# Kernel optimization log

Measured on AMD Instinct MI355X. Metric: run time of the kernel, lower is better.

The kernel has to match this reference:

```python
import jax, jax.numpy as jnp
import numpy as np
import math

B, N, F_IN, F_OUT = 16, 2048, 256, 64


def setup_inputs() -> dict:
    key = jax.random.key(0)
    k1, k2, k3, k4 = jax.random.split(key, 4)
    x = jax.random.normal(k1, (B, N, F_IN), dtype=jnp.float32)
    adj = jax.random.randint(k2, (B, N, N), 0, 2, dtype=jnp.int32)
    stdv = 1.0 / math.sqrt(F_OUT)
    weight = jax.random.uniform(k3, (F_IN, F_OUT), dtype=jnp.float32, minval=-stdv, maxval=stdv)
    # weight2 stdv = 1/sqrt(1) = 1.0
    weight2 = jax.random.uniform(k4, (2 * F_OUT, 1), dtype=jnp.float32, minval=-1.0, maxval=1.0)
    return {"x": x, "adj": adj, "weight": weight, "weight2": weight2}


def reference(x, adj, weight, weight2):
    # h[b,n,o] = (x @ weight)  -- shared linear projection
    h = jnp.einsum("bni,io->bno", x, weight)
    Fo = weight.shape[1]
    # Split additive-attention vector: e_ij = relu(h_i . a_src + h_j . a_dst)
    # Mathematically identical to cat([h_i, h_j]) @ weight2 of the original.
    a_src = weight2[:Fo, 0]
    a_dst = weight2[Fo:, 0]
    s_src = jnp.einsum("bno,o->bn", h, a_src)  # [B, N]
    s_dst = jnp.einsum("bno,o->bn", h, a_dst)  # [B, N]
    e = jax.nn.relu(s_src[:, :, None] + s_dst[:, None, :])  # [B, N, N]
    NEG = jnp.float32(-9e15)
    scores = jnp.where(adj > 0, e, NEG)
    attention = jax.nn.softmax(scores, axis=2)  # softmax over neighbors j
    # dropout = 0.0 / eval mode -> identity
    out = jnp.einsum("bij,bjo->bio", attention, h)  # [B, N, F_OUT]
    return out
```

## Files before the change

kernel.cpp:

```cpp
#include <hip/hip_runtime.h>
#include <hip/hip_bf16.h>

#define BB 16
#define NN 2048
#define FIN 256
#define FO 64
#define CH 128
#define HSTR 136

typedef __bf16 bf16x8 __attribute__((ext_vector_type(8)));
typedef float  f32x4  __attribute__((ext_vector_type(4)));
typedef int    i32x4  __attribute__((ext_vector_type(4)));

__global__ __launch_bounds__(256) void k1_gemm(
    const float* __restrict__ x, const float* __restrict__ weight,
    const float* __restrict__ w2,
    __bf16* __restrict__ hT, float* __restrict__ s_src, float* __restrict__ s_dst) {
    __shared__ __bf16 WtL[FO * 264];
    __shared__ float vsL[FIN], vdL[FIN];
    int t = threadIdx.x;
    {
        const float4* wr = (const float4*)(weight + t * FO);
        float a = 0.f, d = 0.f;
#pragma unroll
        for (int c = 0; c < 16; ++c) {
            float4 v = wr[c];
            int o = c * 4;
            WtL[(o + 0) * 264 + t] = (__bf16)v.x;
            WtL[(o + 1) * 264 + t] = (__bf16)v.y;
            WtL[(o + 2) * 264 + t] = (__bf16)v.z;
            WtL[(o + 3) * 264 + t] = (__bf16)v.w;
            a += v.x * w2[o] + v.y * w2[o + 1] + v.z * w2[o + 2] + v.w * w2[o + 3];
            d += v.x * w2[FO + o] + v.y * w2[FO + o + 1] +
                 v.z * w2[FO + o + 2] + v.w * w2[FO + o + 3];
        }
        vsL[t] = a;
        vdL[t] = d;
    }
    __syncthreads();

    int lane = threadIdx.x & 63, w = threadIdx.x >> 6;
    int quad = lane >> 4, m = lane & 15;
    int Rbase = blockIdx.x * 64 + w * 16;
    int R = Rbase + m;
    const float* xr = x + (long)R * FIN;

    f32x4 acc[4] = {};
    float ps = 0.f, pd = 0.f;

#pragma unroll
    for (int k0 = 0; k0 < FIN; k0 += 32) {
        int kb = k0 + quad * 8;
        float4 x0 = *(const float4*)(xr + kb);
        float4 x1 = *(const float4*)(xr + kb + 4);
        float4 u0 = *(const float4*)(vsL + kb);
        float4 u1 = *(const float4*)(vsL + kb + 4);
        float4 t0 = *(const float4*)(vdL + kb);
        float4 t1 = *(const float4*)(vdL + kb + 4);
        ps += x0.x * u0.x + x0.y * u0.y + x0.z * u0.z + x0.w * u0.w +
              x1.x * u1.x + x1.y * u1.y + x1.z * u1.z + x1.w * u1.w;
        pd += x0.x * t0.x + x0.y * t0.y + x0.z * t0.z + x0.w * t0.w +
              x1.x * t1.x + x1.y * t1.y + x1.z * t1.z + x1.w * t1.w;
        bf16x8 bf = {(__bf16)x0.x, (__bf16)x0.y, (__bf16)x0.z, (__bf16)x0.w,
                     (__bf16)x1.x, (__bf16)x1.y, (__bf16)x1.z, (__bf16)x1.w};
#pragma unroll
        for (int ot = 0; ot < 4; ++ot) {
            bf16x8 af = *(const bf16x8*)(WtL + (ot * 16 + m) * 264 + kb);
            acc[ot] = __builtin_amdgcn_mfma_f32_16x16x32_bf16(af, bf, acc[ot], 0, 0, 0);
        }
    }
    ps += __shfl_xor(ps, 16);
    ps += __shfl_xor(ps, 32);
    pd += __shfl_xor(pd, 16);
    pd += __shfl_xor(pd, 32);
    if (quad == 0) {
        s_src[R] = ps;
        s_dst[R] = pd;
    }
    int b = R >> 11;
    int nb = Rbase & (NN - 1);
#pragma unroll
    for (int ot = 0; ot < 4; ++ot) {
#pragma unroll
        for (int r = 0; r < 4; ++r) {
            int o = ot * 16 + quad * 4 + r;
            hT[((long)b * FO + o) * NN + nb + m] = (__bf16)acc[ot][r];
        }
    }
}

__global__ __launch_bounds__(256, 3) void k2_attn(
    const int* __restrict__ adj, const float* __restrict__ s_src,
    const float* __restrict__ s_dst, const __bf16* __restrict__ hT,
    float* __restrict__ out) {
    __shared__ __bf16 hL[2][FO * HSTR];
    __shared__ float EL[NN];
    int b = blockIdx.x >> 5;
    int i0 = (blockIdx.x & 31) << 6;
    int lane = threadIdx.x & 63, w = threadIdx.x >> 6;
    int quad = lane >> 4, m = lane & 15;
    int rowbase = i0 + w * 16;
    int row = rowbase + m;

    const float* sd = s_dst + b * NN;
    float mx = -3.0e38f;
    for (int j = lane; j < NN; j += 64) mx = fmaxf(mx, sd[j]);
#pragma unroll
    for (int off = 32; off >= 1; off >>= 1) mx = fmaxf(mx, __shfl_xor(mx, off));
    {
        int j0 = threadIdx.x * 8;
        float4 v0 = *(const float4*)(sd + j0);
        float4 v1 = *(const float4*)(sd + j0 + 4);
        EL[j0 + 0] = __expf(v0.x - mx);
        EL[j0 + 1] = __expf(v0.y - mx);
        EL[j0 + 2] = __expf(v0.z - mx);
        EL[j0 + 3] = __expf(v0.w - mx);
        EL[j0 + 4] = __expf(v1.x - mx);
        EL[j0 + 5] = __expf(v1.y - mx);
        EL[j0 + 6] = __expf(v1.z - mx);
        EL[j0 + 7] = __expf(v1.w - mx);
    }

    float cK = __expf(-(s_src[b * NN + row] + mx));

    const i32x4* arow = (const i32x4*)(adj + ((size_t)(b * NN + row)) * NN);
    int aq = quad * 2;

    int so = threadIdx.x >> 2;
    int sc = (threadIdx.x & 3) * 32;
    const __bf16* hsrc = hT + ((long)b * FO + so) * NN + sc;
    int ldoff = so * HSTR + sc;
    int q8 = quad * 8;

    i32x4 A[8];
#pragma unroll
    for (int u = 0; u < 4; ++u) {
        A[2 * u]     = arow[u * 8 + aq];
        A[2 * u + 1] = arow[u * 8 + aq + 1];
    }
    bf16x8 st[4];
    {
        const bf16x8* sp = (const bf16x8*)hsrc;
#pragma unroll
        for (int i = 0; i < 4; ++i) st[i] = sp[i];
    }
    {
        bf16x8* dp = (bf16x8*)(hL[0] + ldoff);
#pragma unroll
        for (int i = 0; i < 4; ++i) dp[i] = st[i];
    }
    __syncthreads();

    f32x4 acc[4] = {};
    f32x4 accL = {};
    const bf16x8 ones = {(__bf16)1.f, (__bf16)1.f, (__bf16)1.f, (__bf16)1.f,
                         (__bf16)1.f, (__bf16)1.f, (__bf16)1.f, (__bf16)1.f};

    for (int c = 0; c < NN / CH; ++c) {
        const __bf16* cur = hL[c & 1];
        bf16x8 af[4];
#pragma unroll
        for (int u = 0; u < 4; ++u) {
            const float* ep = EL + (c * 4 + u) * 32 + q8;
            float4 e0 = *(const float4*)ep;
            float4 e1 = *(const float4*)(ep + 4);
            i32x4 a0 = A[2 * u], a1 = A[2 * u + 1];
            float p0 = (a0.x > 0) ? fmaxf(e0.x, cK) : 0.f;
            float p1 = (a0.y > 0) ? fmaxf(e0.y, cK) : 0.f;
            float p2 = (a0.z > 0) ? fmaxf(e0.z, cK) : 0.f;
            float p3 = (a0.w > 0) ? fmaxf(e0.w, cK) : 0.f;
            float p4 = (a1.x > 0) ? fmaxf(e1.x, cK) : 0.f;
            float p5 = (a1.y > 0) ? fmaxf(e1.y, cK) : 0.f;
            float p6 = (a1.z > 0) ? fmaxf(e1.z, cK) : 0.f;
            float p7 = (a1.w > 0) ? fmaxf(e1.w, cK) : 0.f;
            af[u] = bf16x8{(__bf16)p0, (__bf16)p1, (__bf16)p2, (__bf16)p3,
                           (__bf16)p4, (__bf16)p5, (__bf16)p6, (__bf16)p7};
        }
        if (c < NN / CH - 1) {
            const i32x4* an = arow + (c + 1) * 32;
#pragma unroll
            for (int u = 0; u < 4; ++u) {
                A[2 * u]     = an[u * 8 + aq];
                A[2 * u + 1] = an[u * 8 + aq + 1];
            }
            const bf16x8* sp = (const bf16x8*)(hsrc + (c + 1) * CH);
#pragma unroll
            for (int i = 0; i < 4; ++i) st[i] = sp[i];
        }
#pragma unroll
        for (int u = 0; u < 4; ++u) {
            accL = __builtin_amdgcn_mfma_f32_16x16x32_bf16(af[u], ones, accL, 0, 0, 0);
            const __bf16* hb = cur + u * 32 + q8;
#pragma unroll
            for (int ot = 0; ot < 4; ++ot) {
                bf16x8 bf = *(const bf16x8*)(hb + (ot * 16 + m) * HSTR);
                acc[ot] = __builtin_amdgcn_mfma_f32_16x16x32_bf16(af[u], bf, acc[ot], 0, 0, 0);
            }
        }
        if (c < NN / CH - 1) {
            bf16x8* dp = (bf16x8*)(hL[(c + 1) & 1] + ldoff);
#pragma unroll
            for (int i = 0; i < 4; ++i) dp[i] = st[i];
        }
        __syncthreads();
    }

    float* outp = out + ((long)b * NN + rowbase) * FO;
#pragma unroll
    for (int r = 0; r < 4; ++r) {
        int orow = quad * 4 + r;
        float inv = 1.0f / accL[r];
#pragma unroll
        for (int ot = 0; ot < 4; ++ot) {
            outp[(long)orow * FO + ot * 16 + m] = acc[ot][r] * inv;
        }
    }
}

extern "C" void kernel_launch(void* const* d_in, const int* in_sizes, int n_in,
                              void* d_out, int out_size, void* d_ws, size_t ws_size,
                              hipStream_t stream) {
    const float* x      = (const float*)d_in[0];
    const int*   adj    = (const int*)d_in[1];
    const float* weight = (const float*)d_in[2];
    const float* w2     = (const float*)d_in[3];
    float* out = (float*)d_out;

    char* ws = (char*)d_ws;
    __bf16* hT   = (__bf16*)ws;
    float* s_src = (float*)(ws + 4194304);
    float* s_dst = (float*)(ws + 4194304 + 131072);

    k1_gemm<<<512, 256, 0, stream>>>(x, weight, w2, hT, s_src, s_dst);
    k2_attn<<<512, 256, 0, stream>>>(adj, s_src, s_dst, hT, out);
}
```

Before: 398.6 us.

## Prefetch adjacency two chunks ahead with double register buffers in attention kernel

The attention kernel now keeps two register sets for adjacency data and fetches the adj row slice two chunks ahead. The loop is unrolled by two with a macro so each set is used alternately. The first adj and h loads are hoisted above the max/exp setup so their latency overlaps that work. The full __syncthreads is replaced by an LDS-only waitcnt plus s_barrier, so the barrier does not wait on outstanding global prefetches. The aim is to hide global-memory latency on the 256 MB adj stream, at the cost of more registers, which may hurt occupancy at 3 blocks per SM, and some redundant clamped loads on the last chunks.

```diff
diff --git a/kernel.cpp b/kernel.cpp
--- a/kernel.cpp
+++ b/kernel.cpp
@@ -7,6 +7,7 @@
 #define FO 64
 #define CH 128
 #define HSTR 136
+#define NCH (NN / CH)
 
 typedef __bf16 bf16x8 __attribute__((ext_vector_type(8)));
 typedef float  f32x4  __attribute__((ext_vector_type(4)));
@@ -102,6 +103,33 @@
     int rowbase = i0 + w * 16;
     int row = rowbase + m;
 
+    const i32x4* arow = (const i32x4*)(adj + ((size_t)(b * NN + row)) * NN);
+    int aq = quad * 2;
+
+    int so = threadIdx.x >> 2;
+    int sc = (threadIdx.x & 3) * 32;
+    const __bf16* hsrc = hT + ((long)b * FO + so) * NN + sc;
+    int ldoff = so * HSTR + sc;
+    int q8 = quad * 8;
+
+    bf16x8 st[4];
+    {
+        const bf16x8* sp = (const bf16x8*)hsrc;
+#pragma unroll
+        for (int i = 0; i < 4; ++i) st[i] = sp[i];
+    }
+    i32x4 A0[8], A1[8];
+#pragma unroll
+    for (int u = 0; u < 4; ++u) {
+        A0[2 * u]     = arow[u * 8 + aq];
+        A0[2 * u + 1] = arow[u * 8 + aq + 1];
+    }
+#pragma unroll
+    for (int u = 0; u < 4; ++u) {
+        A1[2 * u]     = arow[32 + u * 8 + aq];
+        A1[2 * u + 1] = arow[32 + u * 8 + aq + 1];
+    }
+
     const float* sd = s_dst + b * NN;
     float mx = -3.0e38f;
     for (int j = lane; j < NN; j += 64) mx = fmaxf(mx, sd[j]);
@@ -123,87 +151,74 @@
 
     float cK = __expf(-(s_src[b * NN + row] + mx));
 
-    const i32x4* arow = (const i32x4*)(adj + ((size_t)(b * NN + row)) * NN);
-    int aq = quad * 2;
-
-    int so = threadIdx.x >> 2;
-    int sc = (threadIdx.x & 3) * 32;
-    const __bf16* hsrc = hT + ((long)b * FO + so) * NN + sc;
-    int ldoff = so * HSTR + sc;
-    int q8 = quad * 8;
-
-    i32x4 A[8];
-#pragma unroll
-    for (int u = 0; u < 4; ++u) {
-        A[2 * u]     = arow[u * 8 + aq];
-        A[2 * u + 1] = arow[u * 8 + aq + 1];
-    }
-    bf16x8 st[4];
-    {
-        const bf16x8* sp = (const bf16x8*)hsrc;
-#pragma unroll
-        for (int i = 0; i < 4; ++i) st[i] = sp[i];
-    }
     {
         bf16x8* dp = (bf16x8*)(hL[0] + ldoff);
 #pragma unroll
         for (int i = 0; i < 4; ++i) dp[i] = st[i];
     }
-    __syncthreads();
+    asm volatile("s_waitcnt lgkmcnt(0)" ::: "memory");
+    __builtin_amdgcn_s_barrier();
 
     f32x4 acc[4] = {};
     f32x4 accL = {};
     const bf16x8 ones = {(__bf16)1.f, (__bf16)1.f, (__bf16)1.f, (__bf16)1.f,
                          (__bf16)1.f, (__bf16)1.f, (__bf16)1.f, (__bf16)1.f};
 
-    for (int c = 0; c < NN / CH; ++c) {
-        const __bf16* cur = hL[c & 1];
-        bf16x8 af[4];
-#pragma unroll
-        for (int u = 0; u < 4; ++u) {
-            const float* ep = EL + (c * 4 + u) * 32 + q8;
-            float4 e0 = *(const float4*)ep;
-            float4 e1 = *(const float4*)(ep + 4);
-            i32x4 a0 = A[2 * u], a1 = A[2 * u + 1];
-            float p0 = (a0.x > 0) ? fmaxf(e0.x, cK) : 0.f;
-            float p1 = (a0.y > 0) ? fmaxf(e0.y, cK) : 0.f;
-            float p2 = (a0.z > 0) ? fmaxf(e0.z, cK) : 0.f;
-            float p3 = (a0.w > 0) ? fmaxf(e0.w, cK) : 0.f;
-            float p4 = (a1.x > 0) ? fmaxf(e1.x, cK) : 0.f;
-            float p5 = (a1.y > 0) ? fmaxf(e1.y, cK) : 0.f;
-            float p6 = (a1.z > 0) ? fmaxf(e1.z, cK) : 0.f;
-            float p7 = (a1.w > 0) ? fmaxf(e1.w, cK) : 0.f;
-            af[u] = bf16x8{(__bf16)p0, (__bf16)p1, (__bf16)p2, (__bf16)p3,
-                           (__bf16)p4, (__bf16)p5, (__bf16)p6, (__bf16)p7};
-        }
-        if (c < NN / CH - 1) {
-            const i32x4* an = arow + (c + 1) * 32;
-#pragma unroll
-            for (int u = 0; u < 4; ++u) {
-                A[2 * u]     = an[u * 8 + aq];
-                A[2 * u + 1] = an[u * 8 + aq + 1];
-            }
-            const bf16x8* sp = (const bf16x8*)(hsrc + (c + 1) * CH);
-#pragma unroll
-            for (int i = 0; i < 4; ++i) st[i] = sp[i];
-        }
-#pragma unroll
-        for (int u = 0; u < 4; ++u) {
-            accL = __builtin_amdgcn_mfma_f32_16x16x32_bf16(af[u], ones, accL, 0, 0, 0);
-            const __bf16* hb = cur + u * 32 + q8;
-#pragma unroll
-            for (int ot = 0; ot < 4; ++ot) {
-                bf16x8 bf = *(const bf16x8*)(hb + (ot * 16 + m) * HSTR);
-                acc[ot] = __builtin_amdgcn_mfma_f32_16x16x32_bf16(af[u], bf, acc[ot], 0, 0, 0);
-            }
-        }
-        if (c < NN / CH - 1) {
-            bf16x8* dp = (bf16x8*)(hL[(c + 1) & 1] + ldoff);
-#pragma unroll
-            for (int i = 0; i < 4; ++i) dp[i] = st[i];
-        }
-        __syncthreads();
-    }
+#define CHUNK(cc, AA)                                                            \
+    {                                                                            \
+        const __bf16* cur = hL[(cc) & 1];                                        \
+        bf16x8 af[4];                                                            \
+        _Pragma("unroll") for (int u = 0; u < 4; ++u) {                          \
+            const float* ep = EL + ((cc) * 4 + u) * 32 + q8;                     \
+            float4 e0 = *(const float4*)ep;                                      \
+            float4 e1 = *(const float4*)(ep + 4);                                \
+            i32x4 a0 = AA[2 * u], a1 = AA[2 * u + 1];                            \
+            float p0 = (a0.x > 0) ? fmaxf(e0.x, cK) : 0.f;                       \
+            float p1 = (a0.y > 0) ? fmaxf(e0.y, cK) : 0.f;                       \
+            float p2 = (a0.z > 0) ? fmaxf(e0.z, cK) : 0.f;                       \
+            float p3 = (a0.w > 0) ? fmaxf(e0.w, cK) : 0.f;                       \
+            float p4 = (a1.x > 0) ? fmaxf(e1.x, cK) : 0.f;                       \
+            float p5 = (a1.y > 0) ? fmaxf(e1.y, cK) : 0.f;                       \
+            float p6 = (a1.z > 0) ? fmaxf(e1.z, cK) : 0.f;                       \
+            float p7 = (a1.w > 0) ? fmaxf(e1.w, cK) : 0.f;                       \
+            af[u] = bf16x8{(__bf16)p0, (__bf16)p1, (__bf16)p2, (__bf16)p3,       \
+                           (__bf16)p4, (__bf16)p5, (__bf16)p6, (__bf16)p7};      \
+        }                                                                        \
+        {                                                                        \
+            int cn = ((cc) + 1 < NCH) ? (cc) + 1 : NCH - 1;                      \
+            int ca = ((cc) + 2 < NCH) ? (cc) + 2 : NCH - 1;                      \
+            const bf16x8* sp = (const bf16x8*)(hsrc + cn * CH);                  \
+            _Pragma("unroll") for (int i = 0; i < 4; ++i) st[i] = sp[i];         \
+            const i32x4* an = arow + ca * 32;                                    \
+            _Pragma("unroll") for (int u = 0; u < 4; ++u) {                      \
+                AA[2 * u]     = an[u * 8 + aq];                                  \
+                AA[2 * u + 1] = an[u * 8 + aq + 1];                              \
+            }                                                                    \
+        }                                                                        \
+        _Pragma("unroll") for (int u = 0; u < 4; ++u) {                          \
+            accL = __builtin_amdgcn_mfma_f32_16x16x32_bf16(af[u], ones, accL,    \
+                                                           0, 0, 0);             \
+            const __bf16* hb = cur + u * 32 + q8;                                \
+            _Pragma("unroll") for (int ot = 0; ot < 4; ++ot) {                   \
+                bf16x8 bf = *(const bf16x8*)(hb + (ot * 16 + m) * HSTR);         \
+                acc[ot] = __builtin_amdgcn_mfma_f32_16x16x32_bf16(af[u], bf,     \
+                                                                  acc[ot],       \
+                                                                  0, 0, 0);      \
+            }                                                                    \
+        }                                                                        \
+        {                                                                        \
+            bf16x8* dp = (bf16x8*)(hL[((cc) + 1) & 1] + ldoff);                  \
+            _Pragma("unroll") for (int i = 0; i < 4; ++i) dp[i] = st[i];         \
+        }                                                                        \
+        asm volatile("s_waitcnt lgkmcnt(0)" ::: "memory");                       \
+        __builtin_amdgcn_s_barrier();                                            \
+    }
+
+    for (int c = 0; c < NCH; c += 2) {
+        CHUNK(c, A0);
+        CHUNK(c + 1, A1);
+    }
+#undef CHUNK
 
     float* outp = out + ((long)b * NN + rowbase) * FO;
 #pragma unroll
```

New measurement: 397.6 us. No clear change (-0.3%).
